# Performance work log

Hardware: AMD Instinct MI355X
Metric: run time of the kernel (lower is better)

The kernel has to match this reference:

```python
import jax, jax.numpy as jnp
import numpy as np

EMBED_DIM = 1024
NUM_HEADS = 16
HEAD_DIM = EMBED_DIM // NUM_HEADS
BATCH = 4
SEQ = 2048


def setup_inputs() -> dict:
    key = jax.random.key(0)
    ks = jax.random.split(key, 9)
    s = 1.0 / np.sqrt(EMBED_DIM)
    x = jax.random.normal(ks[0], (BATCH, SEQ, EMBED_DIM), dtype=jnp.float32)
    # torch.nn.Linear stores weight as [out, in]; y = x @ W.T + b
    Wq = jax.random.uniform(ks[1], (EMBED_DIM, EMBED_DIM), jnp.float32, -s, s)
    bq = jax.random.uniform(ks[2], (EMBED_DIM,), jnp.float32, -s, s)
    Wk = jax.random.uniform(ks[3], (EMBED_DIM, EMBED_DIM), jnp.float32, -s, s)
    bk = jax.random.uniform(ks[4], (EMBED_DIM,), jnp.float32, -s, s)
    Wv = jax.random.uniform(ks[5], (EMBED_DIM, EMBED_DIM), jnp.float32, -s, s)
    bv = jax.random.uniform(ks[6], (EMBED_DIM,), jnp.float32, -s, s)
    Wo = jax.random.uniform(ks[7], (EMBED_DIM, EMBED_DIM), jnp.float32, -s, s)
    bo = jax.random.uniform(ks[8], (EMBED_DIM,), jnp.float32, -s, s)
    return {"x": x, "Wq": Wq, "bq": bq, "Wk": Wk, "bk": bk,
            "Wv": Wv, "bv": bv, "Wo": Wo, "bo": bo}


def reference(x, Wq, bq, Wk, bk, Wv, bv, Wo, bo):
    B, S, E = x.shape
    H, D = NUM_HEADS, HEAD_DIM
    # projections (torch Linear: x @ W.T + b), split heads -> [B, H, S, D]
    q = (x @ Wq.T + bq).reshape(B, S, H, D).transpose(0, 2, 1, 3)
    k = (x @ Wk.T + bk).reshape(B, S, H, D).transpose(0, 2, 1, 3)
    v = (x @ Wv.T + bv).reshape(B, S, H, D).transpose(0, 2, 1, 3)
    scale = 1.0 / np.sqrt(D).astype(np.float32)
    scores = jnp.einsum('bhqd,bhkd->bhqk', q, k) * scale  # [B,H,S,S]
    causal = jnp.tril(jnp.ones((S, S), dtype=bool))
    scores = jnp.where(causal, scores, jnp.float32(-jnp.inf))
    attn = jax.nn.softmax(scores, axis=-1)
    o = jnp.einsum('bhqk,bhkd->bhqd', attn, v)  # [B,H,S,D]
    o = o.transpose(0, 2, 1, 3).reshape(B, S, E)
    return o @ Wo.T + bo
```

## Files before the change

### kernel.cpp

```cpp
#include <hip/hip_runtime.h>
#include <hip/hip_bf16.h>
#include <stdint.h>

#define B_ 4
#define S_ 2048
#define E_ 1024
#define H_ 16
#define D_ 64
#define N_ (B_*S_)

typedef __attribute__((ext_vector_type(4))) float f32x4;
typedef __attribute__((ext_vector_type(8))) short short8;

__device__ __forceinline__ ushort f2bf(float f) {
  uint32_t u = __float_as_uint(f);
  u += 0x7FFF + ((u >> 16) & 1);
  return (ushort)(u >> 16);
}

__device__ __forceinline__ void gload_lds16(const void* g, void* l) {
  __builtin_amdgcn_global_load_lds((const __attribute__((address_space(1))) uint32_t*)g,
                                   (__attribute__((address_space(3))) uint32_t*)l,
                                   16, 0, 0);
}

__global__ void cast_bf16_kernel(const float* __restrict__ in,
                                 ushort* __restrict__ out, int n4) {
  int i = blockIdx.x * blockDim.x + threadIdx.x;
  if (i >= n4) return;
  float4 f = ((const float4*)in)[i];
  ushort4 o;
  o.x = f2bf(f.x); o.y = f2bf(f.y); o.z = f2bf(f.z); o.w = f2bf(f.w);
  ((ushort4*)out)[i] = o;
}

template<int EPI>
__global__ __launch_bounds__(256)
void gemm_bt(const ushort* __restrict__ A, const ushort* __restrict__ Bw,
             const float* __restrict__ bias, void* __restrict__ Cout) {
  __shared__ ushort lA[128*64];
  __shared__ ushort lB[128*64];
  const int t = threadIdx.x;
  const int lane = t & 63;
  const int wave = t >> 6;
  const int wr = wave >> 1, wc = wave & 1;
  const int g = lane >> 4, li = lane & 15;
  const int row0 = blockIdx.x * 128, col0 = blockIdx.y * 128;

  const ushort* Ab = A + (size_t)row0 * E_;
  const ushort* Bb = Bw + (size_t)col0 * E_;

  f32x4 acc[4][4] = {};

  for (int kt = 0; kt < E_; kt += 64) {
    __syncthreads();
    for (int i = 0; i < 4; ++i) {
      int id = i*256 + t;
      int r  = id >> 3;
      int c  = (id & 7) * 8;
      gload_lds16(Ab + (size_t)r*E_ + kt + c, (char*)lA + (i*256 + wave*64)*16);
      gload_lds16(Bb + (size_t)r*E_ + kt + c, (char*)lB + (i*256 + wave*64)*16);
    }
    __syncthreads();
    for (int ks = 0; ks < 2; ++ks) {
      const int ko = ks*32 + g*8;
      short8 af[4], bf[4];
      for (int mi = 0; mi < 4; ++mi)
        af[mi] = *(const short8*)&lA[(wr*64 + mi*16 + li)*64 + ko];
      for (int ni = 0; ni < 4; ++ni)
        bf[ni] = *(const short8*)&lB[(wc*64 + ni*16 + li)*64 + ko];
      for (int mi = 0; mi < 4; ++mi)
        for (int ni = 0; ni < 4; ++ni)
          acc[mi][ni] = __builtin_amdgcn_mfma_f32_16x16x32_bf16(
                            af[mi], bf[ni], acc[mi][ni], 0, 0, 0);
    }
  }

  for (int mi = 0; mi < 4; ++mi)
    for (int ni = 0; ni < 4; ++ni) {
      const int ccol = col0 + wc*64 + ni*16 + li;
      const float bv = bias[ccol];
      const int r0 = row0 + wr*64 + mi*16 + g*4;
      if (EPI == 1) {
        int b = r0 >> 11, s = r0 & (S_-1), h = ccol >> 6, d = ccol & 63;
        ushort4 pk;
        pk.x = f2bf(acc[mi][ni][0] + bv);
        pk.y = f2bf(acc[mi][ni][1] + bv);
        pk.z = f2bf(acc[mi][ni][2] + bv);
        pk.w = f2bf(acc[mi][ni][3] + bv);
        *(ushort4*)&((ushort*)Cout)[((((size_t)b*H_ + h)*D_ + d) << 11) + s] = pk;
      } else {
        for (int j = 0; j < 4; ++j) {
          const int r = r0 + j;
          const float v = acc[mi][ni][j] + bv;
          if (EPI == 0) {
            int b = r >> 11, s = r & (S_-1), h = ccol >> 6, d = ccol & 63;
            ((ushort*)Cout)[((((size_t)b*H_ + h)*S_ + s) << 6) + d] = f2bf(v);
          } else {
            ((float*)Cout)[(size_t)r*E_ + ccol] = v;
          }
        }
      }
    }
}

__global__ __launch_bounds__(256)
void attn_kernel(const ushort* __restrict__ q, const ushort* __restrict__ k,
                 const ushort* __restrict__ vt, ushort* __restrict__ ao) {
  const int qb = blockIdx.x;
  const int bh = blockIdx.y;
  const int b = bh >> 4, h = bh & 15;
  const int t = threadIdx.x, lane = t & 63, wave = t >> 6;
  const int g = lane >> 4, li = lane & 15;
  const int qrow0 = qb*128 + wave*32;

  __shared__ ushort lK[64*72];
  __shared__ ushort lV[64*72];
  __shared__ ushort lP[4][16*72];

  const ushort* qp = q  + (size_t)bh * S_ * D_;
  const ushort* kp = k  + (size_t)bh * S_ * D_;
  const ushort* vp = vt + (size_t)bh * D_ * S_;

  short8 qf[2][2];
  for (int mq = 0; mq < 2; ++mq)
    for (int ks = 0; ks < 2; ++ks)
      qf[mq][ks] = *(const short8*)&qp[(size_t)(qrow0 + mq*16 + li)*D_ + ks*32 + g*8];

  f32x4 o[2][4] = {};
  float m_i[2] = {-3e38f, -3e38f};
  float l_i[2] = {0.f, 0.f};

  const int sr = t >> 2;
  const int sc = (t & 3) * 16;

  short8 rK0, rK1, rV0, rV1;
  rK0 = *(const short8*)&kp[(size_t)sr*D_ + sc];
  rK1 = *(const short8*)&kp[(size_t)sr*D_ + sc + 8];
  rV0 = *(const short8*)&vp[(size_t)sr*S_ + sc];
  rV1 = *(const short8*)&vp[(size_t)sr*S_ + sc + 8];

  const int nkt = 2*qb + 2;
  for (int kt = 0; kt < nkt; ++kt) {
    const int k0 = kt * 64;
    __syncthreads();
    *(short8*)&lK[sr*72 + sc]     = rK0;
    *(short8*)&lK[sr*72 + sc + 8] = rK1;
    *(short8*)&lV[sr*72 + sc]     = rV0;
    *(short8*)&lV[sr*72 + sc + 8] = rV1;
    __syncthreads();
    if (kt + 1 < nkt) {
      const int kn = k0 + 64;
      rK0 = *(const short8*)&kp[(size_t)(kn + sr)*D_ + sc];
      rK1 = *(const short8*)&kp[(size_t)(kn + sr)*D_ + sc + 8];
      rV0 = *(const short8*)&vp[(size_t)sr*S_ + kn + sc];
      rV1 = *(const short8*)&vp[(size_t)sr*S_ + kn + sc + 8];
    }

    if (k0 > qrow0 + 31) continue;

    f32x4 st[2][4] = {};
    for (int ks = 0; ks < 2; ++ks)
      for (int ct = 0; ct < 4; ++ct) {
        short8 kf = *(const short8*)&lK[(ct*16 + li)*72 + ks*32 + g*8];
        st[0][ct] = __builtin_amdgcn_mfma_f32_16x16x32_bf16(kf, qf[0][ks], st[0][ct], 0,0,0);
        st[1][ct] = __builtin_amdgcn_mfma_f32_16x16x32_bf16(kf, qf[1][ks], st[1][ct], 0,0,0);
      }

    for (int mq = 0; mq < 2; ++mq) {
      if (k0 > qrow0 + mq*16 + 15) continue;
      const int qrow = qrow0 + mq*16 + li;
      float mx = -3e38f;
      for (int ct = 0; ct < 4; ++ct)
        for (int j = 0; j < 4; ++j) {
          const int kk = k0 + ct*16 + g*4 + j;
          float x = st[mq][ct][j] * 0.125f;
          x = (kk <= qrow) ? x : -3e38f;
          st[mq][ct][j] = x;
          mx = fmaxf(mx, x);
        }
      mx = fmaxf(mx, __shfl_xor(mx, 16, 64));
      mx = fmaxf(mx, __shfl_xor(mx, 32, 64));
      const float mn = fmaxf(m_i[mq], mx);
      const float alpha = __expf(m_i[mq] - mn);
      m_i[mq] = mn;
      float rs = 0.f;
      for (int ct = 0; ct < 4; ++ct) {
        float p0 = __expf(st[mq][ct][0] - mn);
        float p1 = __expf(st[mq][ct][1] - mn);
        float p2 = __expf(st[mq][ct][2] - mn);
        float p3 = __expf(st[mq][ct][3] - mn);
        rs += (p0 + p1) + (p2 + p3);
        uint32_t w0 = (uint32_t)f2bf(p0) | ((uint32_t)f2bf(p1) << 16);
        uint32_t w1 = (uint32_t)f2bf(p2) | ((uint32_t)f2bf(p3) << 16);
        *(uint32_t*)&lP[wave][li*72 + ct*16 + g*4]     = w0;
        *(uint32_t*)&lP[wave][li*72 + ct*16 + g*4 + 2] = w1;
      }
      rs += __shfl_xor(rs, 16, 64);
      rs += __shfl_xor(rs, 32, 64);
      l_i[mq] = l_i[mq]*alpha + rs;
      for (int dt = 0; dt < 4; ++dt)
        for (int j = 0; j < 4; ++j) o[mq][dt][j] *= alpha;
      for (int ks2 = 0; ks2 < 2; ++ks2) {
        short8 pf = *(const short8*)&lP[wave][li*72 + ks2*32 + g*8];
        for (int dt = 0; dt < 4; ++dt) {
          short8 vf = *(const short8*)&lV[(dt*16 + li)*72 + ks2*32 + g*8];
          o[mq][dt] = __builtin_amdgcn_mfma_f32_16x16x32_bf16(vf, pf, o[mq][dt], 0,0,0);
        }
      }
    }
  }

  for (int mq = 0; mq < 2; ++mq) {
    const float inv_l = 1.0f / l_i[mq];
    const int row = qrow0 + mq*16 + li;
    for (int dt = 0; dt < 4; ++dt) {
      ushort4 pk;
      pk.x = f2bf(o[mq][dt][0] * inv_l);
      pk.y = f2bf(o[mq][dt][1] * inv_l);
      pk.z = f2bf(o[mq][dt][2] * inv_l);
      pk.w = f2bf(o[mq][dt][3] * inv_l);
      *(ushort4*)&ao[((size_t)b*S_ + row)*E_ + h*D_ + dt*16 + g*4] = pk;
    }
  }
}

extern "C" void kernel_launch(void* const* d_in, const int* in_sizes, int n_in,
                              void* d_out, int out_size, void* d_ws, size_t ws_size,
                              hipStream_t stream) {
  (void)in_sizes; (void)n_in; (void)out_size; (void)ws_size;
  const float* x  = (const float*)d_in[0];
  const float* Wq = (const float*)d_in[1];
  const float* bq = (const float*)d_in[2];
  const float* Wk = (const float*)d_in[3];
  const float* bk = (const float*)d_in[4];
  const float* Wv = (const float*)d_in[5];
  const float* bv = (const float*)d_in[6];
  const float* Wo = (const float*)d_in[7];
  const float* bo = (const float*)d_in[8];
  float* out = (float*)d_out;

  char* ws = (char*)d_ws;
  ushort* xb  = (ushort*)(ws);
  ushort* wqb = (ushort*)(ws + 16777216);
  ushort* wkb = (ushort*)(ws + 18874368);
  ushort* wvb = (ushort*)(ws + 20971520);
  ushort* wob = (ushort*)(ws + 23068672);
  ushort* qb_ = (ushort*)(ws + 25165824);
  ushort* kb_ = (ushort*)(ws + 41943040);
  ushort* vtb = (ushort*)(ws + 58720256);
  ushort* aob = xb;

  cast_bf16_kernel<<<8192, 256, 0, stream>>>(x,  xb,  N_*E_/4);
  cast_bf16_kernel<<<1024, 256, 0, stream>>>(Wq, wqb, E_*E_/4);
  cast_bf16_kernel<<<1024, 256, 0, stream>>>(Wk, wkb, E_*E_/4);
  cast_bf16_kernel<<<1024, 256, 0, stream>>>(Wv, wvb, E_*E_/4);
  cast_bf16_kernel<<<1024, 256, 0, stream>>>(Wo, wob, E_*E_/4);

  dim3 gg(N_/128, E_/128);
  gemm_bt<0><<<gg, 256, 0, stream>>>(xb, wqb, bq, qb_);
  gemm_bt<0><<<gg, 256, 0, stream>>>(xb, wkb, bk, kb_);
  gemm_bt<1><<<gg, 256, 0, stream>>>(xb, wvb, bv, vtb);

  attn_kernel<<<dim3(S_/128, B_*H_), 256, 0, stream>>>(qb_, kb_, vtb, aob);

  gemm_bt<2><<<gg, 256, 0, stream>>>(aob, wob, bo, out);
}
```

Before: 394.1 us.

## Balance causal attention work by pairing query tiles and use lazy softmax rescaling

Each attention block now processes a low and a mirrored high 64-row query tile, so every block does a similar amount of causal work, and the grid shrinks to 16 blocks per head. The softmax scale and log2(e) are folded into the Q projection epilogue so the kernel can use exp2 directly. The running-max rescale of the output and denominator is skipped unless the new max exceeds the old one by more than a threshold. Probabilities are packed with a hardware bf16 pack instruction. The lazy rescale lets exponent values grow up to 2^8, which costs some headroom, and having fewer blocks lowers occupancy.

```diff
diff --git a/kernel.cpp b/kernel.cpp
--- a/kernel.cpp
+++ b/kernel.cpp
@@ -37,7 +37,8 @@
 template<int EPI>
 __global__ __launch_bounds__(256)
 void gemm_bt(const ushort* __restrict__ A, const ushort* __restrict__ Bw,
-             const float* __restrict__ bias, void* __restrict__ Cout) {
+             const float* __restrict__ bias, void* __restrict__ Cout,
+             float oscale) {
   __shared__ ushort lA[128*64];
   __shared__ ushort lB[128*64];
   const int t = threadIdx.x;
@@ -84,15 +85,15 @@
       if (EPI == 1) {
         int b = r0 >> 11, s = r0 & (S_-1), h = ccol >> 6, d = ccol & 63;
         ushort4 pk;
-        pk.x = f2bf(acc[mi][ni][0] + bv);
-        pk.y = f2bf(acc[mi][ni][1] + bv);
-        pk.z = f2bf(acc[mi][ni][2] + bv);
-        pk.w = f2bf(acc[mi][ni][3] + bv);
+        pk.x = f2bf((acc[mi][ni][0] + bv) * oscale);
+        pk.y = f2bf((acc[mi][ni][1] + bv) * oscale);
+        pk.z = f2bf((acc[mi][ni][2] + bv) * oscale);
+        pk.w = f2bf((acc[mi][ni][3] + bv) * oscale);
         *(ushort4*)&((ushort*)Cout)[((((size_t)b*H_ + h)*D_ + d) << 11) + s] = pk;
       } else {
         for (int j = 0; j < 4; ++j) {
           const int r = r0 + j;
-          const float v = acc[mi][ni][j] + bv;
+          const float v = (acc[mi][ni][j] + bv) * oscale;
           if (EPI == 0) {
             int b = r >> 11, s = r & (S_-1), h = ccol >> 6, d = ccol & 63;
             ((ushort*)Cout)[((((size_t)b*H_ + h)*S_ + s) << 6) + d] = f2bf(v);
@@ -107,12 +108,13 @@
 __global__ __launch_bounds__(256)
 void attn_kernel(const ushort* __restrict__ q, const ushort* __restrict__ k,
                  const ushort* __restrict__ vt, ushort* __restrict__ ao) {
-  const int qb = blockIdx.x;
+  const int qpair = blockIdx.x;
   const int bh = blockIdx.y;
   const int b = bh >> 4, h = bh & 15;
   const int t = threadIdx.x, lane = t & 63, wave = t >> 6;
   const int g = lane >> 4, li = lane & 15;
-  const int qrow0 = qb*128 + wave*32;
+  const int qlo0 = qpair*64      + wave*16;
+  const int qhi0 = (31-qpair)*64 + wave*16;
 
   __shared__ ushort lK[64*72];
   __shared__ ushort lV[64*72];
@@ -123,9 +125,10 @@
   const ushort* vp = vt + (size_t)bh * D_ * S_;
 
   short8 qf[2][2];
-  for (int mq = 0; mq < 2; ++mq)
-    for (int ks = 0; ks < 2; ++ks)
-      qf[mq][ks] = *(const short8*)&qp[(size_t)(qrow0 + mq*16 + li)*D_ + ks*32 + g*8];
+  for (int ks = 0; ks < 2; ++ks) {
+    qf[0][ks] = *(const short8*)&qp[(size_t)(qlo0 + li)*D_ + ks*32 + g*8];
+    qf[1][ks] = *(const short8*)&qp[(size_t)(qhi0 + li)*D_ + ks*32 + g*8];
+  }
 
   f32x4 o[2][4] = {};
   float m_i[2] = {-3e38f, -3e38f};
@@ -140,7 +143,7 @@
   rV0 = *(const short8*)&vp[(size_t)sr*S_ + sc];
   rV1 = *(const short8*)&vp[(size_t)sr*S_ + sc + 8];
 
-  const int nkt = 2*qb + 2;
+  const int nkt = 32 - qpair;
   for (int kt = 0; kt < nkt; ++kt) {
     const int k0 = kt * 64;
     __syncthreads();
@@ -157,50 +160,56 @@
       rV1 = *(const short8*)&vp[(size_t)sr*S_ + kn + sc + 8];
     }
 
-    if (k0 > qrow0 + 31) continue;
+    const bool do_lo = (k0 <= qlo0 + 15);
 
     f32x4 st[2][4] = {};
     for (int ks = 0; ks < 2; ++ks)
       for (int ct = 0; ct < 4; ++ct) {
         short8 kf = *(const short8*)&lK[(ct*16 + li)*72 + ks*32 + g*8];
-        st[0][ct] = __builtin_amdgcn_mfma_f32_16x16x32_bf16(kf, qf[0][ks], st[0][ct], 0,0,0);
         st[1][ct] = __builtin_amdgcn_mfma_f32_16x16x32_bf16(kf, qf[1][ks], st[1][ct], 0,0,0);
+        if (do_lo)
+          st[0][ct] = __builtin_amdgcn_mfma_f32_16x16x32_bf16(kf, qf[0][ks], st[0][ct], 0,0,0);
       }
 
     for (int mq = 0; mq < 2; ++mq) {
-      if (k0 > qrow0 + mq*16 + 15) continue;
-      const int qrow = qrow0 + mq*16 + li;
+      if (mq == 0 && !do_lo) continue;
+      const int qrow = ((mq == 0) ? qlo0 : qhi0) + li;
       float mx = -3e38f;
       for (int ct = 0; ct < 4; ++ct)
         for (int j = 0; j < 4; ++j) {
           const int kk = k0 + ct*16 + g*4 + j;
-          float x = st[mq][ct][j] * 0.125f;
+          float x = st[mq][ct][j];
           x = (kk <= qrow) ? x : -3e38f;
           st[mq][ct][j] = x;
           mx = fmaxf(mx, x);
         }
       mx = fmaxf(mx, __shfl_xor(mx, 16, 64));
       mx = fmaxf(mx, __shfl_xor(mx, 32, 64));
-      const float mn = fmaxf(m_i[mq], mx);
-      const float alpha = __expf(m_i[mq] - mn);
-      m_i[mq] = mn;
+      if (__any(mx > m_i[mq] + 8.0f)) {
+        const float mn = fmaxf(m_i[mq], mx);
+        const float alpha = exp2f(m_i[mq] - mn);
+        m_i[mq] = mn;
+        l_i[mq] *= alpha;
+        for (int dt = 0; dt < 4; ++dt)
+          for (int j = 0; j < 4; ++j) o[mq][dt][j] *= alpha;
+      }
+      const float mcur = m_i[mq];
       float rs = 0.f;
       for (int ct = 0; ct < 4; ++ct) {
-        float p0 = __expf(st[mq][ct][0] - mn);
-        float p1 = __expf(st[mq][ct][1] - mn);
-        float p2 = __expf(st[mq][ct][2] - mn);
-        float p3 = __expf(st[mq][ct][3] - mn);
+        float p0 = exp2f(st[mq][ct][0] - mcur);
+        float p1 = exp2f(st[mq][ct][1] - mcur);
+        float p2 = exp2f(st[mq][ct][2] - mcur);
+        float p3 = exp2f(st[mq][ct][3] - mcur);
         rs += (p0 + p1) + (p2 + p3);
-        uint32_t w0 = (uint32_t)f2bf(p0) | ((uint32_t)f2bf(p1) << 16);
-        uint32_t w1 = (uint32_t)f2bf(p2) | ((uint32_t)f2bf(p3) << 16);
+        uint32_t w0, w1;
+        asm("v_cvt_pk_bf16_f32 %0, %1, %2" : "=v"(w0) : "v"(p0), "v"(p1));
+        asm("v_cvt_pk_bf16_f32 %0, %1, %2" : "=v"(w1) : "v"(p2), "v"(p3));
         *(uint32_t*)&lP[wave][li*72 + ct*16 + g*4]     = w0;
         *(uint32_t*)&lP[wave][li*72 + ct*16 + g*4 + 2] = w1;
       }
       rs += __shfl_xor(rs, 16, 64);
       rs += __shfl_xor(rs, 32, 64);
-      l_i[mq] = l_i[mq]*alpha + rs;
-      for (int dt = 0; dt < 4; ++dt)
-        for (int j = 0; j < 4; ++j) o[mq][dt][j] *= alpha;
+      l_i[mq] += rs;
       for (int ks2 = 0; ks2 < 2; ++ks2) {
         short8 pf = *(const short8*)&lP[wave][li*72 + ks2*32 + g*8];
         for (int dt = 0; dt < 4; ++dt) {
@@ -213,7 +222,7 @@
 
   for (int mq = 0; mq < 2; ++mq) {
     const float inv_l = 1.0f / l_i[mq];
-    const int row = qrow0 + mq*16 + li;
+    const int row = ((mq == 0) ? qlo0 : qhi0) + li;
     for (int dt = 0; dt < 4; ++dt) {
       ushort4 pk;
       pk.x = f2bf(o[mq][dt][0] * inv_l);
@@ -257,12 +266,13 @@
   cast_bf16_kernel<<<1024, 256, 0, stream>>>(Wv, wvb, E_*E_/4);
   cast_bf16_kernel<<<1024, 256, 0, stream>>>(Wo, wob, E_*E_/4);
 
+  const float QSCALE = 0.125f * 1.44269504f;
   dim3 gg(N_/128, E_/128);
-  gemm_bt<0><<<gg, 256, 0, stream>>>(xb, wqb, bq, qb_);
-  gemm_bt<0><<<gg, 256, 0, stream>>>(xb, wkb, bk, kb_);
-  gemm_bt<1><<<gg, 256, 0, stream>>>(xb, wvb, bv, vtb);
-
-  attn_kernel<<<dim3(S_/128, B_*H_), 256, 0, stream>>>(qb_, kb_, vtb, aob);
-
-  gemm_bt<2><<<gg, 256, 0, stream>>>(aob, wob, bo, out);
-}
+  gemm_bt<0><<<gg, 256, 0, stream>>>(xb, wqb, bq, qb_, QSCALE);
+  gemm_bt<0><<<gg, 256, 0, stream>>>(xb, wkb, bk, kb_, 1.0f);
+  gemm_bt<1><<<gg, 256, 0, stream>>>(xb, wvb, bv, vtb, 1.0f);
+
+  attn_kernel<<<dim3(16, B_*H_), 256, 0, stream>>>(qb_, kb_, vtb, aob);
+
+  gemm_bt<2><<<gg, 256, 0, stream>>>(aob, wob, bo, out, 1.0f);
+}
```

Measured after the change: 334.8 us. 1.18x faster.
